# Optimization experiments

Measured on AMD Instinct MI355X. Metric: run time of the kernel, lower is better.

## Reference

```python
import jax, jax.numpy as jnp
import numpy as np
import math

B, L, DIM = 2, 2048, 1024
HEADS = 16
DH = DIM // HEADS  # 64
M_IALSH = 2
U_IALSH = 0.75
NEG = -1e4  # additive mask value for non-matching hash buckets


def setup_inputs() -> dict:
    key = jax.random.key(0)
    k0, k1, k2, k3 = jax.random.split(key, 4)
    return {
        "hidden_states": jax.random.normal(k0, (B, L, DIM), jnp.float32),
        "qk_w": jax.random.normal(k1, (DIM, DIM), jnp.float32) * 0.02,
        "qk_b": jnp.zeros((DIM,), jnp.float32),
        "v_w": jax.random.normal(k2, (DIM, DIM), jnp.float32) * 0.02,
        "v_b": jnp.zeros((DIM,), jnp.float32),
        "hash_a": jax.random.normal(k3, (DH + M_IALSH,), jnp.float32),
    }


def _ialsh_mask(qkh, hash_a):
    # qkh: (b, h, l, dh). IALSH (Improved Asymmetric LSH for MIPS):
    # keys scaled so max norm per (b,h) is U; P(x)=[x, 1/2-||x||^2, 1/2-||x||^4]
    # queries unit-normalized;        Q(x)=[x/||x||, 0, 0]
    norms = jnp.linalg.norm(qkh, axis=-1, keepdims=True)          # (b,h,l,1)
    max_norm = jnp.max(norms, axis=2, keepdims=True)              # (b,h,1,1)
    xk = qkh * (U_IALSH / jnp.maximum(max_norm, 1e-12))
    nk2 = jnp.sum(xk * xk, axis=-1, keepdims=True)                # ||x||^2
    P = jnp.concatenate([xk, 0.5 - nk2, 0.5 - nk2 * nk2], axis=-1)
    q_unit = qkh / jnp.maximum(norms, 1e-12)
    zeros = jnp.zeros_like(nk2)
    Q = jnp.concatenate([q_unit, zeros, zeros], axis=-1)
    hq = (Q @ hash_a) >= 0.0                                      # (b,h,l) sign hash
    hk = (P @ hash_a) >= 0.0
    same = hq[..., :, None] == hk[..., None, :]                   # (b,h,l,l)
    return jnp.where(same, 0.0, NEG).astype(qkh.dtype)


def reference(hidden_states, qk_w, qk_b, v_w, v_b, hash_a):
    b, l, d = hidden_states.shape
    qk = hidden_states @ qk_w.T + qk_b                            # shared Q/K projection
    v = hidden_states @ v_w.T + v_b

    def split(x):  # (b,l,d) -> (b,h,l,dh)
        return x.reshape(b, l, HEADS, DH).transpose(0, 2, 1, 3)

    qkh, vh = split(qk), split(v)
    scores = jnp.einsum('bhqd,bhkd->bhqk', qkh, qkh) / math.sqrt(DH)
    scores = scores + _ialsh_mask(qkh, hash_a)
    probs = jax.nn.softmax(scores, axis=-1)  # dropout = identity (eval mode)
    ctx = jnp.einsum('bhqk,bhkd->bhqd', probs, vh)
    return ctx.transpose(0, 2, 1, 3).reshape(b, l, d)
```

## Files before the change

### kernel.cpp

```cpp
#include <hip/hip_runtime.h>

typedef unsigned short u16;
typedef unsigned char  u8;
typedef unsigned int   u32;
typedef unsigned long long u64;

typedef short bf16x8 __attribute__((ext_vector_type(8)));
typedef float f32x4  __attribute__((ext_vector_type(4)));
typedef float f32x16 __attribute__((ext_vector_type(16)));

#define DEV __device__ __forceinline__

#if __has_builtin(__builtin_amdgcn_exp2f)
#define EXP2(x) __builtin_amdgcn_exp2f(x)
#else
#define EXP2(x) exp2f(x)
#endif

DEV u16 f2bf(float x) {
  u32 u = __builtin_bit_cast(u32, x);
  u32 r = (u + 0x7fffu + ((u >> 16) & 1u)) >> 16;
  return (u16)r;
}
DEV float bf2f(u16 h) {
  u32 u = ((u32)h) << 16;
  return __builtin_bit_cast(float, u);
}
DEV f32x4 mfma16(bf16x8 a, bf16x8 b, f32x4 c) {
  return __builtin_amdgcn_mfma_f32_16x16x32_bf16(a, b, c, 0, 0, 0);
}
DEV f32x16 mfma32(bf16x8 a, bf16x8 b, f32x16 c) {
  return __builtin_amdgcn_mfma_f32_32x32x16_bf16(a, b, c, 0, 0, 0);
}
DEV u32 cvtpk(float lo, float hi) {
  u32 r;
  asm("v_cvt_pk_bf16_f32 %0, %1, %2" : "=v"(r) : "v"(lo), "v"(hi));
  return r;
}
DEV void pswap(u32& x, u32& y) {
  asm("v_permlane32_swap_b32 %0, %1" : "+v"(x), "+v"(y));
}
DEV bf16x8 mkfrag(u32 w0, u32 w1, u32 w2, u32 w3) {
  union { u32 w[4]; bf16x8 v; } u;
  u.w[0] = w0; u.w[1] = w1; u.w[2] = w2; u.w[3] = w3;
  return u.v;
}

#define GLDS(gptr, lptr)                                                  \
  __builtin_amdgcn_global_load_lds(                                       \
      (const __attribute__((address_space(1))) void*)(gptr),              \
      (__attribute__((address_space(3))) void*)(lptr), 16, 0, 0)

__global__ __launch_bounds__(256) void split3_kernel(
    const float* __restrict__ hid, const float* __restrict__ wq,
    const float* __restrict__ wv,
    u16* __restrict__ hHi, u16* __restrict__ hLo,
    u16* __restrict__ wqHi, u16* __restrict__ wqLo, u16* __restrict__ wvHi) {
  const int NH4 = 1048576, NW4 = 262144;
  int i = blockIdx.x * 256 + threadIdx.x;
  if (i < NH4) {
    float4 v = ((const float4*)hid)[i];
    ushort4 h, l;
    h.x = f2bf(v.x); l.x = f2bf(v.x - bf2f(h.x));
    h.y = f2bf(v.y); l.y = f2bf(v.y - bf2f(h.y));
    h.z = f2bf(v.z); l.z = f2bf(v.z - bf2f(h.z));
    h.w = f2bf(v.w); l.w = f2bf(v.w - bf2f(h.w));
    ((ushort4*)hHi)[i] = h;
    ((ushort4*)hLo)[i] = l;
  } else if (i < NH4 + NW4) {
    int j = i - NH4;
    float4 v = ((const float4*)wq)[j];
    ushort4 h, l;
    h.x = f2bf(v.x); l.x = f2bf(v.x - bf2f(h.x));
    h.y = f2bf(v.y); l.y = f2bf(v.y - bf2f(h.y));
    h.z = f2bf(v.z); l.z = f2bf(v.z - bf2f(h.z));
    h.w = f2bf(v.w); l.w = f2bf(v.w - bf2f(h.w));
    ((ushort4*)wqHi)[j] = h;
    ((ushort4*)wqLo)[j] = l;
  } else {
    int j = i - NH4 - NW4;
    float4 v = ((const float4*)wv)[j];
    ushort4 h;
    h.x = f2bf(v.x); h.y = f2bf(v.y); h.z = f2bf(v.z); h.w = f2bf(v.w);
    ((ushort4*)wvHi)[j] = h;
  }
}

__global__ __launch_bounds__(256) void ca_kernel(
    const float* __restrict__ W, const float* __restrict__ ha, double* __restrict__ ca) {
  int idx = blockIdx.x * 256 + threadIdx.x;
  int h = idx >> 10, k = idx & 1023;
  double s = 0.0;
#pragma unroll 8
  for (int j = 0; j < 64; ++j)
    s += (double)W[(size_t)(h * 64 + j) * 1024 + k] * (double)ha[j];
  ca[idx] = s;
}

__global__ __launch_bounds__(256) void d_kernel(
    const float* __restrict__ hid, const double* __restrict__ ca, float* __restrict__ dq) {
  const int row0 = blockIdx.x * 8 + (threadIdx.x >> 6) * 2;
  const int lane = threadIdx.x & 63;
  double a0[16], a1[16];
#pragma unroll
  for (int h = 0; h < 16; ++h) { a0[h] = 0.0; a1[h] = 0.0; }
  const float* hp = hid + (size_t)row0 * 1024;
  for (int k = lane; k < 1024; k += 64) {
    const double h0 = (double)hp[k];
    const double h1 = (double)hp[k + 1024];
#pragma unroll
    for (int h = 0; h < 16; ++h) {
      const double c = ca[h * 1024 + k];
      a0[h] += h0 * c;
      a1[h] += h1 * c;
    }
  }
#pragma unroll
  for (int h = 0; h < 16; ++h) {
    double v0 = a0[h], v1 = a1[h];
#pragma unroll
    for (int off = 32; off; off >>= 1) {
      v0 += __shfl_xor(v0, off, 64);
      v1 += __shfl_xor(v1, off, 64);
    }
    if (lane == 0) {
      const int b0 = row0 >> 11, l0 = row0 & 2047;
      dq[(size_t)(b0 * 16 + h) * 2048 + l0] = (float)v0;
      const int r1 = row0 + 1;
      dq[(size_t)((r1 >> 11) * 16 + h) * 2048 + (r1 & 2047)] = (float)v1;
    }
  }
}

__global__ __launch_bounds__(256, 2) void gemm_fused(
    const u16* __restrict__ hHi, const u16* __restrict__ hLo,
    const u16* __restrict__ wqHi, const u16* __restrict__ wqLo,
    const u16* __restrict__ wvHi,
    const float* __restrict__ qk_b, const float* __restrict__ v_b,
    u16* __restrict__ qkB, u16* __restrict__ vT, float* __restrict__ n2A) {
  constexpr int K = 1024;
  __shared__ u16 S[2][16384];
  const int tid = threadIdx.x, wave = tid >> 6, lane = tid & 63;
  const int quad = lane >> 4, lm = lane & 15;
  const int wr = wave >> 1, wc = wave & 1;
  const int m0 = blockIdx.x * 64, n0 = blockIdx.y * 128;
  const int ch = lane & 3, rA = lane >> 2;

  auto stage = [&](int kt, int buf) {
    const int k0 = kt * 32;
    const int rowA = wave * 16 + rA;
    GLDS(hHi + (size_t)(m0 + rowA) * K + k0 + ch * 8, &S[buf][0 + wave * 512]);
    GLDS(hLo + (size_t)(m0 + rowA) * K + k0 + ch * 8, &S[buf][2048 + wave * 512]);
#pragma unroll
    for (int it = 0; it < 2; ++it) {
      const int rb = wave * 2 + it;
      const int row = rb * 16 + rA;
      GLDS(wqHi + (size_t)(n0 + row) * K + k0 + ch * 8, &S[buf][4096 + rb * 512]);
      GLDS(wqLo + (size_t)(n0 + row) * K + k0 + ch * 8, &S[buf][8192 + rb * 512]);
      GLDS(wvHi + (size_t)(n0 + row) * K + k0 + ch * 8, &S[buf][12288 + rb * 512]);
    }
  };

  f32x4 aq[2][4], av[4][2];
#pragma unroll
  for (int i = 0; i < 2; ++i)
#pragma unroll
    for (int j = 0; j < 4; ++j) aq[i][j] = {0.f, 0.f, 0.f, 0.f};
#pragma unroll
  for (int i = 0; i < 4; ++i)
#pragma unroll
    for (int j = 0; j < 2; ++j) av[i][j] = {0.f, 0.f, 0.f, 0.f};

  stage(0, 0);
  __syncthreads();

  for (int kt = 0; kt < 32; ++kt) {
    const int cur = kt & 1;
    if (kt < 31) stage(kt + 1, cur ^ 1);

    bf16x8 a_h[2], a_l[2], b_h[4], b_l[4], w_h[4];
#pragma unroll
    for (int i = 0; i < 2; ++i) {
      a_h[i] = *(const bf16x8*)&S[cur][(wr * 32 + i * 16 + lm) * 32 + quad * 8];
      a_l[i] = *(const bf16x8*)&S[cur][2048 + (wr * 32 + i * 16 + lm) * 32 + quad * 8];
    }
#pragma unroll
    for (int j = 0; j < 4; ++j) {
      b_h[j] = *(const bf16x8*)&S[cur][4096 + (wc * 64 + j * 16 + lm) * 32 + quad * 8];
      b_l[j] = *(const bf16x8*)&S[cur][8192 + (wc * 64 + j * 16 + lm) * 32 + quad * 8];
      w_h[j] = *(const bf16x8*)&S[cur][12288 + (wc * 64 + j * 16 + lm) * 32 + quad * 8];
    }
#pragma unroll
    for (int i = 0; i < 2; ++i)
#pragma unroll
      for (int j = 0; j < 4; ++j) {
        aq[i][j] = mfma16(a_h[i], b_h[j], aq[i][j]);
        aq[i][j] = mfma16(a_h[i], b_l[j], aq[i][j]);
        aq[i][j] = mfma16(a_l[i], b_h[j], aq[i][j]);
      }
#pragma unroll
    for (int iv = 0; iv < 4; ++iv)
#pragma unroll
      for (int jv = 0; jv < 2; ++jv)
        av[iv][jv] = mfma16(w_h[iv], a_h[jv], av[iv][jv]);

    __syncthreads();
  }

  const int hidx = blockIdx.y * 2 + wc;
#pragma unroll
  for (int i = 0; i < 2; ++i) {
    float nn[4] = {0.f, 0.f, 0.f, 0.f};
#pragma unroll
    for (int j = 0; j < 4; ++j) {
      const int col = n0 + wc * 64 + j * 16 + lm;
      const float bv = qk_b[col];
#pragma unroll
      for (int r = 0; r < 4; ++r) {
        const int row = m0 + wr * 32 + i * 16 + quad * 4 + r;
        const float val = aq[i][j][r] + bv;
        qkB[(size_t)row * 1024 + col] = f2bf(val);
        nn[r] += val * val;
      }
    }
#pragma unroll
    for (int r = 0; r < 4; ++r)
#pragma unroll
      for (int off = 1; off < 16; off <<= 1) nn[r] += __shfl_xor(nn[r], off, 64);
    if (lm == 0) {
      const int row = m0 + wr * 32 + i * 16 + quad * 4;
      const int b = row >> 11, l = row & 2047;
      *(float4*)&n2A[(size_t)(b * 16 + hidx) * 2048 + l] =
          make_float4(nn[0], nn[1], nn[2], nn[3]);
    }
  }
#pragma unroll
  for (int iv = 0; iv < 4; ++iv)
#pragma unroll
    for (int r = 0; r < 4; ++r) {
      const int vcol = n0 + wc * 64 + iv * 16 + quad * 4 + r;
      const float bv = v_b[vcol];
#pragma unroll
      for (int jv = 0; jv < 2; ++jv) {
        const int tok = m0 + wr * 32 + jv * 16 + lm;
        vT[(size_t)vcol * 4096 + tok] = f2bf(av[iv][jv][r] + bv);
      }
    }
}

__global__ __launch_bounds__(256) void bits_kernel(
    const float* __restrict__ n2A, const float* __restrict__ dq,
    const float* __restrict__ ha, u8* __restrict__ hqA, u64* __restrict__ hkM) {
  const int bh = blockIdx.x;
  const int tid = threadIdx.x;
  const int wave = tid >> 6, lane = tid & 63;
  __shared__ float red[4];
  const float* n2p = n2A + (size_t)bh * 2048;
  float4 v0 = ((const float4*)n2p)[tid];
  float4 v1 = ((const float4*)n2p)[tid + 256];
  float lmax = fmaxf(fmaxf(fmaxf(v0.x, v0.y), fmaxf(v0.z, v0.w)),
                     fmaxf(fmaxf(v1.x, v1.y), fmaxf(v1.z, v1.w)));
#pragma unroll
  for (int off = 1; off < 64; off <<= 1) lmax = fmaxf(lmax, __shfl_xor(lmax, off, 64));
  if (lane == 0) red[wave] = lmax;
  __syncthreads();
  const float maxn2 = fmaxf(fmaxf(red[0], red[1]), fmaxf(red[2], red[3]));
  const float s = 0.75f / fmaxf(sqrtf(maxn2), 1e-12f);
  const float a64 = ha[64], a65 = ha[65];
#pragma unroll
  for (int it = 0; it < 8; ++it) {
    const int l = it * 256 + tid;
    const float dv = dq[(size_t)bh * 2048 + l];
    const float n2 = n2p[l];
    const float nk2 = s * s * n2;
    const float hkdot = s * dv + (0.5f - nk2) * a64 + (0.5f - nk2 * nk2) * a65;
    hqA[(size_t)bh * 2048 + l] = (dv >= 0.f) ? 1 : 0;
    const u64 m = __ballot(hkdot >= 0.f);
    if (lane == 0) hkM[(size_t)bh * 32 + it * 4 + wave] = m;
  }
}

__global__ __launch_bounds__(256, 2) void attn_kernel(
    const u16* __restrict__ qkb, const u16* __restrict__ vT,
    const u8* __restrict__ hqA, const u64* __restrict__ hkM,
    float* __restrict__ out, float* __restrict__ pO1,
    float* __restrict__ pL0, float* __restrict__ pL1) {
  __shared__ u16 Ks[2][4096];
  __shared__ u16 Vs[2][4096];

  const int id = blockIdx.x;
  const int bh = id & 31, qt = (id >> 5) & 15, kz = id >> 9;
  const int b = bh >> 4, h = bh & 15;
  const int tid = threadIdx.x, wave = tid >> 6, lane = tid & 63;
  const int col = lane & 31;
  const int hf = lane >> 5;
  const int ch7 = col & 7;
  const int r8 = lane >> 3, ch = lane & 7;
  const int q0 = qt * 128;
  const int token = q0 + wave * 32 + col;
  const int kts = kz * 16, kte = kts + 16;

  const u16* qbase = qkb + (size_t)b * 2048 * 1024 + h * 64;
  const u16* vtb = vT + (size_t)h * 64 * 4096 + b * 2048;
  const u64* hkp = hkM + (size_t)bh * 32;

  bf16x8 aQ[4];
#pragma unroll
  for (int c = 0; c < 4; ++c)
    aQ[c] = *(const bf16x8*)(qbase + (size_t)token * 1024 + c * 16 + hf * 8);
  const u32 hqx = hqA[(size_t)bh * 2048 + token] ? 0xFFFFFFFFu : 0u;

  const int srow = wave * 16;
  auto stage = [&](int kt, int buf) {
#pragma unroll
    for (int i = 0; i < 2; ++i) {
      const int row = srow + i * 8 + r8;
      const int sw = (ch ^ (row & 7)) * 8;
      GLDS(qbase + (size_t)(kt * 64 + row) * 1024 + sw, &Ks[buf][(srow + i * 8) * 64]);
      GLDS(vtb + (size_t)row * 4096 + kt * 64 + sw, &Vs[buf][(srow + i * 8) * 64]);
    }
  };

  f32x16 acc[2];
#pragma unroll
  for (int d = 0; d < 2; ++d)
#pragma unroll
    for (int r = 0; r < 16; ++r) acc[d][r] = 0.f;
  float accL = 0.f;

  const float SCL = 0.18033688f;
  const float M0 = -4.3280854f;

  u64 mk = hkp[kts];
  stage(kts, 0);
  __syncthreads();

  for (int kt = kts; kt < kte; ++kt) {
    const int cur = kt & 1;
    if (kt + 1 < kte) stage(kt + 1, cur ^ 1);
    const u64 mk_next = (kt + 1 < kte) ? hkp[kt + 1] : 0ull;

    const u64 msh = mk >> (hf * 4);
    u32 mw[2];
    mw[0] = (u32)msh;
    mw[1] = (u32)(msh >> 32);

#pragma unroll
    for (int kb = 0; kb < 2; ++kb) {
      const u32 hw = mw[kb] ^ hqx;
      f32x16 cs;
#pragma unroll
      for (int r = 0; r < 16; ++r) cs[r] = 0.f;
      __builtin_amdgcn_s_setprio(1);
#pragma unroll
      for (int c = 0; c < 4; ++c) {
        const bf16x8 aK = *(const bf16x8*)
            &Ks[cur][(kb * 32 + col) * 64 + (((c * 2 + hf) ^ ch7) * 8)];
        cs = mfma32(aK, aQ[c], cs);
      }
      __builtin_amdgcn_s_setprio(0);

      float pv[16];
#pragma unroll
      for (int r = 0; r < 16; ++r) {
        const int pos = (r & 3) + 8 * (r >> 2);
        float p = EXP2(__builtin_fmaf(cs[r], SCL, M0));
        p = ((hw >> pos) & 1u) ? 0.f : p;
        accL += p;
        pv[r] = p;
      }
      u32 pk[8];
#pragma unroll
      for (int i = 0; i < 8; ++i) pk[i] = cvtpk(pv[2 * i], pv[2 * i + 1]);
      pswap(pk[0], pk[2]);
      pswap(pk[1], pk[3]);
      pswap(pk[4], pk[6]);
      pswap(pk[5], pk[7]);
      const bf16x8 fr0 = mkfrag(pk[0], pk[1], pk[2], pk[3]);
      const bf16x8 fr1 = mkfrag(pk[4], pk[5], pk[6], pk[7]);

      __builtin_amdgcn_s_setprio(1);
#pragma unroll
      for (int db = 0; db < 2; ++db) {
        const bf16x8 aV0 = *(const bf16x8*)
            &Vs[cur][(db * 32 + col) * 64 + ((((kb * 2 + 0) * 2 + hf) ^ ch7) * 8)];
        acc[db] = mfma32(aV0, fr0, acc[db]);
        const bf16x8 aV1 = *(const bf16x8*)
            &Vs[cur][(db * 32 + col) * 64 + ((((kb * 2 + 1) * 2 + hf) ^ ch7) * 8)];
        acc[db] = mfma32(aV1, fr1, acc[db]);
      }
      __builtin_amdgcn_s_setprio(0);
    }

    mk = mk_next;
    __syncthreads();
  }

  accL += __shfl_xor(accL, 32);
  float* obase = kz ? pO1 : out;
  float* lbase = kz ? pL1 : pL0;
  if (hf == 0) lbase[(size_t)bh * 2048 + token] = accL;
  float* op = obase + (size_t)(b * 2048 + token) * 1024 + h * 64 + hf * 4;
#pragma unroll
  for (int db = 0; db < 2; ++db)
#pragma unroll
    for (int g = 0; g < 4; ++g) {
      float4 v4 = make_float4(acc[db][g * 4 + 0], acc[db][g * 4 + 1],
                              acc[db][g * 4 + 2], acc[db][g * 4 + 3]);
      *(float4*)(op + db * 32 + g * 8) = v4;
    }
}

__global__ __launch_bounds__(256) void combine_kernel(
    const float* __restrict__ pO1, const float* __restrict__ pL0,
    const float* __restrict__ pL1, float* __restrict__ out) {
  const int j = blockIdx.x * 256 + threadIdx.x;
  const int row = j >> 8;
  const int h = (j & 255) >> 4;
  const int b = row >> 11, l = row & 2047;
  const size_t li = (size_t)(b * 16 + h) * 2048 + l;
  const float inv = 1.0f / (pL0[li] + pL1[li]);
  const float4 a = ((const float4*)out)[j];
  const float4 c = ((const float4*)pO1)[j];
  ((float4*)out)[j] = make_float4((a.x + c.x) * inv, (a.y + c.y) * inv,
                                  (a.z + c.z) * inv, (a.w + c.w) * inv);
}

extern "C" void kernel_launch(void* const* d_in, const int* in_sizes, int n_in,
                              void* d_out, int out_size, void* d_ws, size_t ws_size,
                              hipStream_t stream) {
  const float* hidden = (const float*)d_in[0];
  const float* qk_w   = (const float*)d_in[1];
  const float* qk_b   = (const float*)d_in[2];
  const float* v_w    = (const float*)d_in[3];
  const float* v_b    = (const float*)d_in[4];
  const float* hash_a = (const float*)d_in[5];
  float* out = (float*)d_out;

  char* base = (char*)d_ws;
  size_t off = 0;
  auto take = [&](size_t bytes) -> char* {
    char* r = base + off;
    off += (bytes + 255) & ~(size_t)255;
    return r;
  };
  const size_t NH = 4194304;
  const size_t NW = 1048576;
  u16* hHi  = (u16*)take(NH * 2);
  u16* hLo  = (u16*)take(NH * 2);
  u16* wqHi = (u16*)take(NW * 2);
  u16* wqLo = (u16*)take(NW * 2);
  u16* wvHi = (u16*)take(NW * 2);
  u16* qkB  = (u16*)take(NH * 2);
  u16* vT   = (u16*)take(NH * 2);
  double* ca = (double*)take(16 * 1024 * 8);
  float* dq  = (float*)take(65536 * 4);
  float* n2A = (float*)take(65536 * 4);
  u8* hqA = (u8*)take(65536);
  u64* hkM = (u64*)take(32 * 32 * 8);

  float* pO1 = (float*)hHi;
  float* pL0 = (float*)wqHi;
  float* pL1 = pL0 + 65536;

  hipLaunchKernelGGL(split3_kernel, dim3(6144), dim3(256), 0, stream,
                     hidden, qk_w, v_w, hHi, hLo, wqHi, wqLo, wvHi);
  hipLaunchKernelGGL(ca_kernel, dim3(64), dim3(256), 0, stream, qk_w, hash_a, ca);
  hipLaunchKernelGGL(d_kernel, dim3(512), dim3(256), 0, stream, hidden, ca, dq);
  hipLaunchKernelGGL(gemm_fused, dim3(64, 8), dim3(256), 0, stream,
                     hHi, hLo, wqHi, wqLo, wvHi, qk_b, v_b, qkB, vT, n2A);
  hipLaunchKernelGGL(bits_kernel, dim3(32), dim3(256), 0, stream, n2A, dq, hash_a, hqA, hkM);
  hipLaunchKernelGGL(attn_kernel, dim3(1024), dim3(256), 0, stream,
                     qkB, vT, hqA, hkM, out, pO1, pL0, pL1);
  hipLaunchKernelGGL(combine_kernel, dim3(4096), dim3(256), 0, stream,
                     pO1, pL0, pL1, out);
}
```

Measured before the change: 224.7 us.

## Process two query groups per wave to reuse K/V fragments in attention

Each wave now handles 64 query tokens as two 32-token groups, so every K and V fragment read from shared memory feeds two MFMAs instead of one. The query tile per block grows from 128 to 256 and the attention grid halves from 1024 to 512 blocks. This is meant to cut LDS read traffic and per-block staging overhead per unit of work. In exchange it roughly doubles the accumulator registers, which may hurt occupancy, and leaves fewer blocks to spread across the GPU's compute units.

Result: no change. 225.3 us (+0.3%).

```diff
diff --git a/kernel.cpp b/kernel.cpp
--- a/kernel.cpp
+++ b/kernel.cpp
@@ -289,26 +289,31 @@
   __shared__ u16 Vs[2][4096];
 
   const int id = blockIdx.x;
-  const int bh = id & 31, qt = (id >> 5) & 15, kz = id >> 9;
+  const int bh = id & 31, qt = (id >> 5) & 7, kz = id >> 8;
   const int b = bh >> 4, h = bh & 15;
   const int tid = threadIdx.x, wave = tid >> 6, lane = tid & 63;
   const int col = lane & 31;
   const int hf = lane >> 5;
   const int ch7 = col & 7;
   const int r8 = lane >> 3, ch = lane & 7;
-  const int q0 = qt * 128;
-  const int token = q0 + wave * 32 + col;
+  const int q0 = qt * 256;
+  const int tok0 = q0 + wave * 64 + col;
   const int kts = kz * 16, kte = kts + 16;
 
   const u16* qbase = qkb + (size_t)b * 2048 * 1024 + h * 64;
   const u16* vtb = vT + (size_t)h * 64 * 4096 + b * 2048;
   const u64* hkp = hkM + (size_t)bh * 32;
 
-  bf16x8 aQ[4];
-#pragma unroll
-  for (int c = 0; c < 4; ++c)
-    aQ[c] = *(const bf16x8*)(qbase + (size_t)token * 1024 + c * 16 + hf * 8);
-  const u32 hqx = hqA[(size_t)bh * 2048 + token] ? 0xFFFFFFFFu : 0u;
+  bf16x8 aQ[2][4];
+  u32 hqx[2];
+#pragma unroll
+  for (int g = 0; g < 2; ++g) {
+#pragma unroll
+    for (int c = 0; c < 4; ++c)
+      aQ[g][c] = *(const bf16x8*)(qbase +
+          (size_t)(tok0 + g * 32) * 1024 + c * 16 + hf * 8);
+    hqx[g] = hqA[(size_t)bh * 2048 + tok0 + g * 32] ? 0xFFFFFFFFu : 0u;
+  }
 
   const int srow = wave * 16;
   auto stage = [&](int kt, int buf) {
@@ -321,12 +326,14 @@
     }
   };
 
-  f32x16 acc[2];
+  f32x16 acc[2][2];
 #pragma unroll
   for (int d = 0; d < 2; ++d)
 #pragma unroll
-    for (int r = 0; r < 16; ++r) acc[d][r] = 0.f;
-  float accL = 0.f;
+    for (int g = 0; g < 2; ++g)
+#pragma unroll
+      for (int r = 0; r < 16; ++r) acc[d][g][r] = 0.f;
+  float accL[2] = {0.f, 0.f};
 
   const float SCL = 0.18033688f;
   const float M0 = -4.3280854f;
@@ -347,47 +354,61 @@
 
 #pragma unroll
     for (int kb = 0; kb < 2; ++kb) {
-      const u32 hw = mw[kb] ^ hqx;
-      f32x16 cs;
-#pragma unroll
-      for (int r = 0; r < 16; ++r) cs[r] = 0.f;
+      bf16x8 aK[4];
+#pragma unroll
+      for (int c = 0; c < 4; ++c)
+        aK[c] = *(const bf16x8*)
+            &Ks[cur][(kb * 32 + col) * 64 + (((c * 2 + hf) ^ ch7) * 8)];
+
+      f32x16 cs0, cs1;
+#pragma unroll
+      for (int r = 0; r < 16; ++r) { cs0[r] = 0.f; cs1[r] = 0.f; }
       __builtin_amdgcn_s_setprio(1);
 #pragma unroll
       for (int c = 0; c < 4; ++c) {
-        const bf16x8 aK = *(const bf16x8*)
-            &Ks[cur][(kb * 32 + col) * 64 + (((c * 2 + hf) ^ ch7) * 8)];
-        cs = mfma32(aK, aQ[c], cs);
+        cs0 = mfma32(aK[c], aQ[0][c], cs0);
+        cs1 = mfma32(aK[c], aQ[1][c], cs1);
       }
       __builtin_amdgcn_s_setprio(0);
 
-      float pv[16];
-#pragma unroll
-      for (int r = 0; r < 16; ++r) {
-        const int pos = (r & 3) + 8 * (r >> 2);
-        float p = EXP2(__builtin_fmaf(cs[r], SCL, M0));
-        p = ((hw >> pos) & 1u) ? 0.f : p;
-        accL += p;
-        pv[r] = p;
-      }
-      u32 pk[8];
-#pragma unroll
-      for (int i = 0; i < 8; ++i) pk[i] = cvtpk(pv[2 * i], pv[2 * i + 1]);
-      pswap(pk[0], pk[2]);
-      pswap(pk[1], pk[3]);
-      pswap(pk[4], pk[6]);
-      pswap(pk[5], pk[7]);
-      const bf16x8 fr0 = mkfrag(pk[0], pk[1], pk[2], pk[3]);
-      const bf16x8 fr1 = mkfrag(pk[4], pk[5], pk[6], pk[7]);
+      bf16x8 fr[2][2];
+#pragma unroll
+      for (int g = 0; g < 2; ++g) {
+        const u32 hw = mw[kb] ^ hqx[g];
+        u32 pk[8];
+#pragma unroll
+        for (int i = 0; i < 8; ++i) {
+          const int r0 = 2 * i, r1 = 2 * i + 1;
+          const int pos0 = (r0 & 3) + 8 * (r0 >> 2);
+          const int pos1 = (r1 & 3) + 8 * (r1 >> 2);
+          const float c0 = (g == 0) ? cs0[r0] : cs1[r0];
+          const float c1 = (g == 0) ? cs0[r1] : cs1[r1];
+          float p0 = EXP2(__builtin_fmaf(c0, SCL, M0));
+          float p1 = EXP2(__builtin_fmaf(c1, SCL, M0));
+          p0 = ((hw >> pos0) & 1u) ? 0.f : p0;
+          p1 = ((hw >> pos1) & 1u) ? 0.f : p1;
+          accL[g] += p0 + p1;
+          pk[i] = cvtpk(p0, p1);
+        }
+        pswap(pk[0], pk[2]);
+        pswap(pk[1], pk[3]);
+        pswap(pk[4], pk[6]);
+        pswap(pk[5], pk[7]);
+        fr[g][0] = mkfrag(pk[0], pk[1], pk[2], pk[3]);
+        fr[g][1] = mkfrag(pk[4], pk[5], pk[6], pk[7]);
+      }
 
       __builtin_amdgcn_s_setprio(1);
 #pragma unroll
       for (int db = 0; db < 2; ++db) {
         const bf16x8 aV0 = *(const bf16x8*)
             &Vs[cur][(db * 32 + col) * 64 + ((((kb * 2 + 0) * 2 + hf) ^ ch7) * 8)];
-        acc[db] = mfma32(aV0, fr0, acc[db]);
+        acc[db][0] = mfma32(aV0, fr[0][0], acc[db][0]);
+        acc[db][1] = mfma32(aV0, fr[1][0], acc[db][1]);
         const bf16x8 aV1 = *(const bf16x8*)
             &Vs[cur][(db * 32 + col) * 64 + ((((kb * 2 + 1) * 2 + hf) ^ ch7) * 8)];
-        acc[db] = mfma32(aV1, fr1, acc[db]);
+        acc[db][0] = mfma32(aV1, fr[0][1], acc[db][0]);
+        acc[db][1] = mfma32(aV1, fr[1][1], acc[db][1]);
       }
       __builtin_amdgcn_s_setprio(0);
     }
@@ -396,19 +417,24 @@
     __syncthreads();
   }
 
-  accL += __shfl_xor(accL, 32);
   float* obase = kz ? pO1 : out;
   float* lbase = kz ? pL1 : pL0;
-  if (hf == 0) lbase[(size_t)bh * 2048 + token] = accL;
-  float* op = obase + (size_t)(b * 2048 + token) * 1024 + h * 64 + hf * 4;
-#pragma unroll
-  for (int db = 0; db < 2; ++db)
-#pragma unroll
-    for (int g = 0; g < 4; ++g) {
-      float4 v4 = make_float4(acc[db][g * 4 + 0], acc[db][g * 4 + 1],
-                              acc[db][g * 4 + 2], acc[db][g * 4 + 3]);
-      *(float4*)(op + db * 32 + g * 8) = v4;
-    }
+#pragma unroll
+  for (int g = 0; g < 2; ++g) {
+    float lg = accL[g];
+    lg += __shfl_xor(lg, 32);
+    const int token = tok0 + g * 32;
+    if (hf == 0) lbase[(size_t)bh * 2048 + token] = lg;
+    float* op = obase + (size_t)(b * 2048 + token) * 1024 + h * 64 + hf * 4;
+#pragma unroll
+    for (int db = 0; db < 2; ++db)
+#pragma unroll
+      for (int gg = 0; gg < 4; ++gg) {
+        float4 v4 = make_float4(acc[db][g][gg * 4 + 0], acc[db][g][gg * 4 + 1],
+                                acc[db][g][gg * 4 + 2], acc[db][g][gg * 4 + 3]);
+        *(float4*)(op + db * 32 + gg * 8) = v4;
+      }
+  }
 }
 
 __global__ __launch_bounds__(256) void combine_kernel(
@@ -470,7 +496,7 @@
   hipLaunchKernelGGL(gemm_fused, dim3(64, 8), dim3(256), 0, stream,
                      hHi, hLo, wqHi, wqLo, wvHi, qk_b, v_b, qkB, vT, n2A);
   hipLaunchKernelGGL(bits_kernel, dim3(32), dim3(256), 0, stream, n2A, dq, hash_a, hqA, hkM);
-  hipLaunchKernelGGL(attn_kernel, dim3(1024), dim3(256), 0, stream,
+  hipLaunchKernelGGL(attn_kernel, dim3(512), dim3(256), 0, stream,
                      qkB, vT, hqA, hkM, out, pO1, pL0, pL1);
   hipLaunchKernelGGL(combine_kernel, dim3(4096), dim3(256), 0, stream,
                      pO1, pL0, pL1, out);
```
